# Optimization experiments

Hardware: AMD Instinct MI355X
Metric: run time of the kernel (lower is better)

The kernel has to match this reference:

```python
import jax, jax.numpy as jnp
import numpy as np

N, G, M = 3000, 1000, 4000  # cells, genes, decoder nodes (M = N + G)


def _gat(A, W, Wb, vt, vtb, vr, vrb, H):
    # One graphattention_layer. Torch recomputes relu(W @ H) three times; the
    # math is identical, so compute it once.
    Z = jax.nn.relu(H @ W.T + Wb)            # (n, out)
    s = (Z @ vt.T + vtb).T                   # (1, n) -- vkt scores
    r = (Z @ vr.T + vrb).T                   # (1, n) -- vkr scores
    Ms = A * s                               # column-wise scaling of A
    Mr = (A * r).T                           # row-wise scaling (transposed)
    Att = jax.nn.softmax(jax.nn.sigmoid(Ms + Mr), axis=-1)  # torch dim=1 default for 2D
    return Att @ Z                           # (n, out)


LAYER_DIMS = {"e1": (N, 512), "e2": (512, 256), "e3": (256, 64),
              "d1": (64, 256), "d2": (256, 512), "d3": (512, M), "d4": (512, G)}


def setup_inputs() -> dict:
    key = jax.random.key(0)
    ks = iter(jax.random.split(key, 64))
    def rn(shape, scale=1.0):
        return jax.random.normal(next(ks), shape, dtype=jnp.float32) * scale
    inp = {}
    inp["X"] = jax.random.uniform(next(ks), (N, N), dtype=jnp.float32)      # cell adjacency (encoder input)
    inp["A_enc"] = jax.random.uniform(next(ks), (N, N), dtype=jnp.float32)  # encoder adjM
    inp["A_dec"] = jax.random.uniform(next(ks), (M, M), dtype=jnp.float32)  # decoder adjM (N+G nodes)
    inp["gG"] = rn((64, G))                                                  # gene embeddings
    for name, (fi, fo) in LAYER_DIMS.items():
        inp[name + "_W"] = rn((fo, fi), 1.0 / np.sqrt(fi))
        inp[name + "_Wb"] = jnp.zeros((fo,), jnp.float32)
        inp[name + "_vt"] = rn((1, fo), 1.0 / np.sqrt(fo))
        inp[name + "_vtb"] = jnp.zeros((1,), jnp.float32)
        inp[name + "_vr"] = rn((1, fo), 1.0 / np.sqrt(fo))
        inp[name + "_vrb"] = jnp.zeros((1,), jnp.float32)
    return inp


def reference(X, A_enc, A_dec, gG,
              e1_W, e1_Wb, e1_vt, e1_vtb, e1_vr, e1_vrb,
              e2_W, e2_Wb, e2_vt, e2_vtb, e2_vr, e2_vrb,
              e3_W, e3_Wb, e3_vt, e3_vtb, e3_vr, e3_vrb,
              d1_W, d1_Wb, d1_vt, d1_vtb, d1_vr, d1_vrb,
              d2_W, d2_Wb, d2_vt, d2_vtb, d2_vr, d2_vrb,
              d3_W, d3_Wb, d3_vt, d3_vtb, d3_vr, d3_vrb,
              d4_W, d4_Wb, d4_vt, d4_vtb, d4_vr, d4_vrb):
    H1 = _gat(A_enc, e1_W, e1_Wb, e1_vt, e1_vtb, e1_vr, e1_vrb, X.T)
    H2 = _gat(A_enc, e2_W, e2_Wb, e2_vt, e2_vtb, e2_vr, e2_vrb, H1)
    H3 = _gat(A_enc, e3_W, e3_Wb, e3_vt, e3_vtb, e3_vr, e3_vrb, H2)
    Henc = H3.T                                  # (64, N)
    # decoder: stack gene embeddings, transpose to (M, 64)
    D = jnp.concatenate([gG, Henc], axis=1).T    # (M, 64)
    D1 = _gat(A_dec, d1_W, d1_Wb, d1_vt, d1_vtb, d1_vr, d1_vrb, D)
    D2 = _gat(A_dec, d2_W, d2_Wb, d2_vt, d2_vtb, d2_vr, d2_vrb, D1)
    cell = _gat(A_dec, d3_W, d3_Wb, d3_vt, d3_vtb, d3_vr, d3_vrb, D2)   # (M, M)
    gene = _gat(A_dec, d4_W, d4_Wb, d4_vt, d4_vtb, d4_vr, d4_vrb, D2)   # (M, G)
    return (cell, gene)
```

## Files before the change

kernel.cpp:

```cpp
#include <hip/hip_runtime.h>
#include <hip/hip_bf16.h>

using bf16 = __hip_bfloat16;
typedef __bf16 bf16x8 __attribute__((ext_vector_type(8)));
typedef __bf16 bf16x4 __attribute__((ext_vector_type(4)));
typedef float f32x4 __attribute__((ext_vector_type(4)));
typedef unsigned short u16x4 __attribute__((ext_vector_type(4)));

#define N_CELLS 3000
#define N_GENES 1000
#define M_NODES 4000
#define NP 3072
#define MP 4096

__device__ __forceinline__ float rdv(const void* p, size_t i, int isbf) {
    if (isbf) return (float)((const bf16*)p)[i];
    return ((const float*)p)[i];
}

__device__ __forceinline__ f32x4 load4g(const void* A, int n, int row, int col, int isbf) {
    f32x4 v = {0.f, 0.f, 0.f, 0.f};
    if (row < n) {
        if (col + 3 < n) {
            if (isbf) {
                const u16x4 u = *(const u16x4*)((const unsigned short*)A + (size_t)row * n + col);
                #pragma unroll
                for (int k = 0; k < 4; k++) v[k] = __uint_as_float(((unsigned)u[k]) << 16);
            } else {
                v = *(const f32x4*)((const float*)A + (size_t)row * n + col);
            }
        } else {
            #pragma unroll
            for (int k = 0; k < 4; k++)
                if (col + k < n) v[k] = rdv(A, (size_t)row * n + col + k, isbf);
        }
    }
    return v;
}

__device__ __forceinline__ f32x4 load4b(const bf16* A, int ld, int row, int col) {
    const u16x4 u = *(const u16x4*)((const unsigned short*)A + (size_t)row * ld + col);
    f32x4 v;
    #pragma unroll
    for (int k = 0; k < 4; k++) v[k] = __uint_as_float(((unsigned)u[k]) << 16);
    return v;
}

__device__ __forceinline__ void async_copy16(const bf16* g, bf16* l) {
    __builtin_amdgcn_global_load_lds((const __attribute__((address_space(1))) void*)g,
                                     (__attribute__((address_space(3))) void*)l,
                                     16, 0, 0);
}

__global__ void sniff_dtype(const unsigned int* __restrict__ X, int* __restrict__ flag)
{
    __shared__ int cnt[4];
    int t = threadIdx.x;
    int c = 0;
    for (int i = t; i < 2048; i += 256)
        if ((X[i] & 0xFFFFu) < 0x3F80u) c++;
    #pragma unroll
    for (int off = 32; off > 0; off >>= 1) c += __shfl_down(c, off);
    if ((t & 63) == 0) cnt[t >> 6] = c;
    __syncthreads();
    if (t == 0) flag[0] = (cnt[0] + cnt[1] + cnt[2] + cnt[3] > 1536) ? 1 : 0;
}

template<bool BIAS_ROW, bool SCALE_ROW, bool ATOMIC, bool SCORES, typename OutT>
__global__ __launch_bounds__(256, 2)
void gemm_nt(const bf16* __restrict__ A, int lda,
             const bf16* __restrict__ B, int ldb,
             const bf16* __restrict__ bias,
             const float* __restrict__ rsum,
             OutT* __restrict__ C, int ldc,
             int K, int mBound, int nBound,
             const void* __restrict__ vtp, const void* __restrict__ vrp,
             const int* __restrict__ flag, int oBase, int oBound,
             float* __restrict__ sAcc, float* __restrict__ rAcc)
{
    __shared__ __align__(16) bf16 As[2][128 * 32];
    __shared__ __align__(16) bf16 Bs[2][128 * 32];
    const int tid  = threadIdx.x;
    const int wave = tid >> 6;
    const int lane = tid & 63;

    const int orig = blockIdx.y * gridDim.x + blockIdx.x;
    int i0, j0;
    if (gridDim.x == 32 && gridDim.y == 32) {
        const int xcd = orig & 7, idx = orig >> 3;
        const int r = ((xcd >> 1) << 3) + (idx >> 4);
        const int c = ((xcd & 1) << 4) + (idx & 15);
        i0 = r * 128;
        j0 = c * 128;
    } else {
        const int nwg = gridDim.x * gridDim.y;
        const int q = nwg >> 3, rr = nwg & 7;
        const int xcd = orig & 7, idx = orig >> 3;
        const int swz = (xcd < rr ? xcd * (q + 1) : rr * (q + 1) + (xcd - rr) * q) + idx;
        i0 = (swz / gridDim.x) * 128;
        j0 = (swz % gridDim.x) * 128;
    }

    const int kSlice = K / gridDim.z;
    const int kBase  = blockIdx.z * kSlice;
    const int kEnd   = kBase + kSlice;

    const int srow = lane >> 2;
    const int sk   = (lane & 3) * 8;
    const bf16* gA0 = A + (size_t)(i0 + wave * 32 + srow) * lda + sk;
    const bf16* gA1 = gA0 + (size_t)16 * lda;
    const bf16* gB0 = B + (size_t)(j0 + wave * 32 + srow) * ldb + sk;
    const bf16* gB1 = gB0 + (size_t)16 * ldb;
    const int loA0 = (wave * 32) * 32;
    const int loA1 = (wave * 32 + 16) * 32;

    const int wm = (wave >> 1) * 64;
    const int wn = (wave & 1) * 64;
    const int fr = lane & 15;
    const int fk = (lane >> 4) * 8;

    f32x4 acc[4][4] = {};

    auto stage = [&](int buf, int kt) {
        async_copy16(gA0 + kt, &As[buf][loA0]);
        async_copy16(gA1 + kt, &As[buf][loA1]);
        async_copy16(gB0 + kt, &Bs[buf][loA0]);
        async_copy16(gB1 + kt, &Bs[buf][loA1]);
    };

    stage(0, kBase);
    __syncthreads();
    int cur = 0;

    for (int kt = kBase; kt < kEnd; kt += 32) {
        if (kt + 32 < kEnd) stage(cur ^ 1, kt + 32);

        bf16x8 af[4], bfv[4];
        #pragma unroll
        for (int t = 0; t < 4; t++) {
            af[t]  = *(const bf16x8*)&As[cur][(wm + t * 16 + fr) * 32 + fk];
            bfv[t] = *(const bf16x8*)&Bs[cur][(wn + t * 16 + fr) * 32 + fk];
        }
        #pragma unroll
        for (int mt = 0; mt < 4; mt++)
            #pragma unroll
            for (int nt = 0; nt < 4; nt++)
                acc[mt][nt] = __builtin_amdgcn_mfma_f32_16x16x32_bf16(
                    af[mt], bfv[nt], acc[mt][nt], 0, 0, 0);

        __syncthreads();
        cur ^= 1;
    }

    const int ci = (lane >> 4) * 4;
    const int cj = lane & 15;
    int isbf = 0;
    if constexpr (SCORES) isbf = flag[0];
    float ps[4] = {0.f, 0.f, 0.f, 0.f};
    float pr[4] = {0.f, 0.f, 0.f, 0.f};
    #pragma unroll
    for (int mt = 0; mt < 4; mt++) {
        #pragma unroll
        for (int rg = 0; rg < 4; rg++) {
            const int gi = i0 + wm + mt * 16 + ci + rg;
            if (gi >= mBound) continue;
            float bv = 0.f, rc = 1.f;
            if (BIAS_ROW) bv = (float)bias[gi];
            if (SCALE_ROW) {
                const float r_ = rsum[gi];
                rc = r_ > 0.f ? __builtin_amdgcn_rcpf(r_) : 0.f;
            }
            float vtv = 0.f, vrv = 0.f;
            if constexpr (SCORES) {
                if (gi < oBound) {
                    vtv = rdv(vtp, (size_t)(oBase + gi), isbf);
                    vrv = rdv(vrp, (size_t)(oBase + gi), isbf);
                }
            }
            #pragma unroll
            for (int nt = 0; nt < 4; nt++) {
                const int gj = j0 + wn + nt * 16 + cj;
                if (gj >= nBound) continue;
                float v = acc[mt][nt][rg];
                if (BIAS_ROW) { v += bv; v = v > 0.f ? v : 0.f; }
                if (SCALE_ROW) v *= rc;
                if constexpr (ATOMIC) {
                    atomicAdd((float*)&C[(size_t)gi * ldc + gj], v);
                } else {
                    C[(size_t)gi * ldc + gj] = (OutT)v;
                }
                if constexpr (SCORES) {
                    ps[nt] += v * vtv;
                    pr[nt] += v * vrv;
                }
            }
        }
    }
    if constexpr (SCORES) {
        #pragma unroll
        for (int nt = 0; nt < 4; nt++) {
            float p = ps[nt], r2 = pr[nt];
            p  += __shfl_down(p, 32);  p  += __shfl_down(p, 16);
            r2 += __shfl_down(r2, 32); r2 += __shfl_down(r2, 16);
            if (lane < 16) {
                const int gj = j0 + wn + nt * 16 + lane;
                if (gj < nBound) {
                    atomicAdd(&sAcc[gj], p);
                    atomicAdd(&rAcc[gj], r2);
                }
            }
        }
    }
}

__global__ void padcopy(const void* __restrict__ src, int r, int c,
                        bf16* __restrict__ dst, int rp, int cp,
                        const int* __restrict__ flag)
{
    const int isbf = flag[0];
    long idx = (long)blockIdx.x * 256 + threadIdx.x;
    if (idx >= (long)rp * cp) return;
    int i = (int)(idx / cp), j = (int)(idx % cp);
    float v = 0.f;
    if (i < r && j < c) v = rdv(src, (size_t)i * c + j, isbf);
    dst[idx] = (bf16)v;
}

struct PadSeg { const void* src; bf16* dst; int r, c, cp; long base; };
struct PadArgs { PadSeg seg[14]; long total; };
__global__ void padcopy_multi(PadArgs a, const int* __restrict__ flag)
{
    const int isbf = flag[0];
    long idx = (long)blockIdx.x * 256 + threadIdx.x;
    const long str = (long)gridDim.x * 256;
    for (; idx < a.total; idx += str) {
        int s = 0;
        #pragma unroll
        for (int k = 1; k < 14; k++) if (idx >= a.seg[k].base) s = k;
        const long loc = idx - a.seg[s].base;
        const int cp = a.seg[s].cp;
        const int i = (int)(loc / cp), j = (int)(loc % cp);
        float v = 0.f;
        if (i < a.seg[s].r && j < a.seg[s].c)
            v = rdv(a.seg[s].src, (size_t)i * a.seg[s].c + j, isbf);
        a.seg[s].dst[loc] = (bf16)v;
    }
}

__global__ void padcopy_T(const void* __restrict__ src, int n,
                          bf16* __restrict__ dst, int np,
                          const int* __restrict__ flag)
{
    __shared__ float t[32][33];
    const int isbf = flag[0];
    const int tx = threadIdx.x & 31;
    const int ty = threadIdx.x >> 5;
    const int i0 = blockIdx.y * 32;
    const int k0 = blockIdx.x * 32;
    #pragma unroll
    for (int q = 0; q < 4; q++) {
        int k = k0 + ty + q * 8;
        float v = 0.f;
        if (k < n && i0 + tx < n) v = rdv(src, (size_t)k * n + i0 + tx, isbf);
        t[ty + q * 8][tx] = v;
    }
    __syncthreads();
    #pragma unroll
    for (int q = 0; q < 4; q++) {
        int i = ty + q * 8;
        dst[(size_t)(i0 + i) * np + k0 + tx] = (bf16)t[tx][i];
    }
}

__global__ void zero_f32(float* __restrict__ p, int n)
{
    int i = blockIdx.x * 256 + threadIdx.x;
    if (i < n) p[i] = 0.f;
}

__global__ void zero_f32v(f32x4* __restrict__ p, long n4)
{
    long i = (long)blockIdx.x * 256 + threadIdx.x;
    const long str = (long)gridDim.x * 256;
    const f32x4 z = {0.f, 0.f, 0.f, 0.f};
    for (; i < n4; i += str) p[i] = z;
}

__global__ void f32_to_bf16_v4(const f32x4* __restrict__ src, bf16x4* __restrict__ dst, long n4)
{
    long i = (long)blockIdx.x * 256 + threadIdx.x;
    const long str = (long)gridDim.x * 256;
    for (; i < n4; i += str) {
        f32x4 v = src[i];
        bf16x4 w;
        #pragma unroll
        for (int k = 0; k < 4; k++) w[k] = (__bf16)v[k];
        dst[i] = w;
    }
}

template<bool CB>
__global__ __launch_bounds__(256)
void e_pass_pair(const void* __restrict__ A, int ldA, int n,
                 const float* __restrict__ s, const float* __restrict__ r,
                 const void* __restrict__ vtb, const void* __restrict__ vrb,
                 bf16* __restrict__ E, int ldE, float* __restrict__ rowsum,
                 const int* __restrict__ flag)
{
    extern __shared__ char smem[];
    const int bi = blockIdx.y, bj = blockIdx.x;
    if (bj < bi) return;
    const int isbf = flag[0];
    const int tid = threadIdx.x;
    const int i0 = bi * 64, j0 = bj * 64;
    const int tx = tid & 15;
    const int ty = tid >> 4;
    const int c0 = 4 * tx;
    const float bt = rdv(vtb, 0, isbf);
    const float br = rdv(vrb, 0, isbf);

    auto ld4 = [&](int row, int col) -> f32x4 {
        if constexpr (CB) return load4b((const bf16*)A, ldA, row, col);
        else              return load4g(A, n, row, col, isbf);
    };
    auto stT = [&](int which, int a, int b, float v) {
        if constexpr (CB) ((__bf16*)smem)[((which << 6) + a) * 66 + b] = (__bf16)v;
        else              ((float*)smem)[((which << 6) + a) * 65 + b] = v;
    };
    auto ldT = [&](int which, int a, int b) -> float {
        if constexpr (CB) return (float)((__bf16*)smem)[((which << 6) + a) * 66 + b];
        else              return ((float*)smem)[((which << 6) + a) * 65 + b];
    };

    #pragma unroll
    for (int rr = 0; rr < 4; rr++) {
        const int rw = ty + 16 * rr;
        f32x4 v1 = ld4(i0 + rw, j0 + c0);
        f32x4 v2 = ld4(j0 + rw, i0 + c0);
        #pragma unroll
        for (int k = 0; k < 4; k++) {
            stT(0, c0 + k, rw, v1[k]);
            stT(1, c0 + k, rw, v2[k]);
        }
    }
    __syncthreads();

    const float LOG2E = 1.442695041f;

    {
        f32x4 s4 = *(const f32x4*)&s[j0 + c0];
        #pragma unroll
        for (int k = 0; k < 4; k++) s4[k] += bt;
        #pragma unroll
        for (int q = 0; q < 4; q++) {
            const int li = ty + 16 * q;
            const int gi = i0 + li;
            const float rv = r[gi] + br;
            const f32x4 a = ld4(gi, j0 + c0);
            f32x4 ev;
            float part = 0.f;
            #pragma unroll
            for (int k = 0; k < 4; k++) {
                const float trn = ldT(1, li, c0 + k);
                const float x = a[k] * s4[k] + trn * rv;
                const float t = __builtin_amdgcn_exp2f(-x * LOG2E);
                const float sig = __builtin_amdgcn_rcpf(1.f + t);
                float e = __builtin_amdgcn_exp2f(sig * LOG2E);
                const int gj = j0 + c0 + k;
                e = (gi < n && gj < n) ? e : 0.f;
                ev[k] = e;
                part += e;
            }
            bf16x4 w;
            #pragma unroll
            for (int k = 0; k < 4; k++) w[k] = (__bf16)ev[k];
            *(bf16x4*)&E[(size_t)gi * ldE + j0 + c0] = w;
            part += __shfl_down(part, 8, 16);
            part += __shfl_down(part, 4, 16);
            part += __shfl_down(part, 2, 16);
            part += __shfl_down(part, 1, 16);
            if (tx == 0) atomicAdd(&rowsum[gi], part);
        }
    }

    if (bj > bi) {
        f32x4 s4 = *(const f32x4*)&s[i0 + c0];
        #pragma unroll
        for (int k = 0; k < 4; k++) s4[k] += bt;
        #pragma unroll
        for (int q = 0; q < 4; q++) {
            const int lr = ty + 16 * q;
            const int gr = j0 + lr;
            const float rv = r[gr] + br;
            const f32x4 a = ld4(gr, i0 + c0);
            f32x4 ev;
            float part = 0.f;
            #pragma unroll
            for (int k = 0; k < 4; k++) {
                const float trn = ldT(0, lr, c0 + k);
                const float x = a[k] * s4[k] + trn * rv;
                const float t = __builtin_amdgcn_exp2f(-x * LOG2E);
                const float sig = __builtin_amdgcn_rcpf(1.f + t);
                float e = __builtin_amdgcn_exp2f(sig * LOG2E);
                const int gj = i0 + c0 + k;
                e = (gr < n && gj < n) ? e : 0.f;
                ev[k] = e;
                part += e;
            }
            bf16x4 w;
            #pragma unroll
            for (int k = 0; k < 4; k++) w[k] = (__bf16)ev[k];
            *(bf16x4*)&E[(size_t)gr * ldE + i0 + c0] = w;
            part += __shfl_down(part, 8, 16);
            part += __shfl_down(part, 4, 16);
            part += __shfl_down(part, 2, 16);
            part += __shfl_down(part, 1, 16);
            if (tx == 0) atomicAdd(&rowsum[gr], part);
        }
    }
}

__global__ void build_D(const void* __restrict__ gG, const bf16* __restrict__ H3,
                        bf16* __restrict__ D, const int* __restrict__ flag)
{
    const int isbf = flag[0];
    int idx = blockIdx.x * 256 + threadIdx.x;
    int m = idx >> 7, c = idx & 127;
    float v = 0.f;
    if (c < 64) {
        if (m < N_GENES)      v = rdv(gG, (size_t)c * N_GENES + m, isbf);
        else if (m < M_NODES) v = (float)H3[(size_t)(m - N_GENES) * 128 + c];
    }
    D[idx] = (bf16)v;
}

extern "C" void kernel_launch(void* const* d_in, const int* in_sizes, int n_in,
                              void* d_out, int out_size, void* d_ws, size_t ws_size,
                              hipStream_t stream)
{
    const void* X     = d_in[0];
    const void* A_enc = d_in[1];
    const void* A_dec = d_in[2];
    const void* gG    = d_in[3];
    const void *W[7], *Wb[7], *vt[7], *vtb[7], *vr[7], *vrb[7];
    for (int l = 0; l < 7; l++) {
        W[l]   = d_in[4 + 6 * l + 0];
        Wb[l]  = d_in[4 + 6 * l + 1];
        vt[l]  = d_in[4 + 6 * l + 2];
        vtb[l] = d_in[4 + 6 * l + 3];
        vr[l]  = d_in[4 + 6 * l + 4];
        vrb[l] = d_in[4 + 6 * l + 5];
    }

    const int fop[7] = {512, 256, 128, 256, 512, 4096, 1024};
    const int fip[7] = {3072, 512, 256, 128, 256, 512, 512};
    const int foR[7] = {512, 256, 64, 256, 512, 4000, 1000};
    const int fiR[7] = {3000, 512, 256, 64, 256, 512, 512};

    const int  CHcap = (ws_size >= (size_t)100 * 1024 * 1024) ? 4096 : 1024;
    const bool useAB = (ws_size >= (size_t)130 * 1024 * 1024);

    char* ws = (char*)d_ws;
    size_t off = 0;
    auto alloc = [&](size_t bytes) -> void* {
        void* p = ws + off;
        off += (bytes + 255) & ~(size_t)255;
        return p;
    };
    int*   flag = (int*)alloc(256);
    float* sb   = (float*)alloc((size_t)MP * 4);
    float* rb   = (float*)alloc((size_t)MP * 4);
    float* rsum = (float*)alloc((size_t)MP * 4);
    bf16* Bp[7];
    for (int l = 0; l < 7; l++) Bp[l] = (bf16*)alloc((size_t)fop[l] * 2);
    bf16* RA = (bf16*)alloc((size_t)NP * 512 * 2);
    bf16* RB = (bf16*)alloc((size_t)NP * 256 * 2);
    bf16* RC = (bf16*)alloc((size_t)MP * 512 * 2);
    bf16 *H1 = RA, *H3 = RA, *D1 = RA;
    bf16 *H2 = RB, *Dd = RB;
    bf16 *D2 = RC;
    bf16* Wp[7];
    for (int l = 0; l < 7; l++) Wp[l] = (bf16*)alloc((size_t)fop[l] * fip[l] * 2);
    float* Hf = (float*)alloc((size_t)MP * 512 * 4);
    bf16*  ZT = (bf16*)alloc((size_t)CHcap * MP * 2);
    bf16*  E  = (bf16*)alloc((size_t)MP * MP * 2);
    bf16*  Ab = useAB ? (bf16*)alloc((size_t)MP * MP * 2) : nullptr;
    bf16* XT = E;

    auto pickS = [](int base, int Kc) -> int {
        if (base >= 192) return 1;
        const int steps = Kc / 32;
        int best = 1;
        for (int S = 1; S <= 16; S++) {
            if (steps % S) continue;
            if (Kc / S < 256) continue;
            if (base * S > 1536) break;
            best = S;
            if (base * S >= 768) break;
        }
        return best;
    };

    sniff_dtype<<<1, 256, 0, stream>>>((const unsigned int*)X, flag);
    {
        PadArgs pa;
        long base = 0;
        for (int l = 0; l < 7; l++) {
            pa.seg[l] = {W[l], Wp[l], foR[l], fiR[l], fip[l], base};
            base += (long)fop[l] * fip[l];
        }
        for (int l = 0; l < 7; l++) {
            pa.seg[7 + l] = {Wb[l], Bp[l], 1, foR[l], fop[l], base};
            base += fop[l];
        }
        pa.total = base;
        padcopy_multi<<<2048, 256, 0, stream>>>(pa, flag);
    }
    padcopy_T<<<dim3(NP / 32, NP / 32), 256, 0, stream>>>(X, N_CELLS, XT, NP, flag);
    if (useAB)
        padcopy<<<dim3((NP * NP) / 256), 256, 0, stream>>>(
            A_enc, N_CELLS, N_CELLS, Ab, NP, NP, flag);

    const unsigned smemCB = 2 * 64 * 66 * 2;
    const unsigned smemF  = 2 * 64 * 65 * 4;

    auto layer = [&](const bf16* Hin, int l, const void* Araw, int nABpad,
                     int nReal, int nPad, bf16* HoutB, float* HoutF,
                     int ldOut, int mB, int nBtot) {
        const int K = fip[l], NO = fop[l];
        const int CH = NO > CHcap ? CHcap : NO;
        const int nch = NO / CH;
        auto gemm1 = [&](int c, bool withScores) {
            int sB = foR[l] - c * CH;
            if (sB > CH) sB = CH;
            if (sB < 0) sB = 0;
            if (withScores)
                gemm_nt<true, false, false, true, bf16><<<dim3(nPad / 128, CH / 128), 256, 0, stream>>>(
                    Wp[l] + (size_t)c * CH * K, K, Hin, K, Bp[l] + c * CH, nullptr,
                    ZT, nPad, K, CH, nPad,
                    vt[l], vr[l], flag, c * CH, sB, sb, rb);
            else
                gemm_nt<true, false, false, false, bf16><<<dim3(nPad / 128, CH / 128), 256, 0, stream>>>(
                    Wp[l] + (size_t)c * CH * K, K, Hin, K, Bp[l] + c * CH, nullptr,
                    ZT, nPad, K, CH, nPad,
                    nullptr, nullptr, nullptr, 0, 0, nullptr, nullptr);
        };
        zero_f32<<<dim3(3 * MP / 256), 256, 0, stream>>>(sb, 3 * MP);
        for (int c = 0; c < nch; c++) gemm1(c, true);
        if (useAB)
            e_pass_pair<true><<<dim3(nPad / 64, nPad / 64), 256, smemCB, stream>>>(
                Ab, nABpad, nReal, sb, rb, vtb[l], vrb[l], E, nPad, rsum, flag);
        else
            e_pass_pair<false><<<dim3(nPad / 64, nPad / 64), 256, smemF, stream>>>(
                Araw, nReal, nReal, sb, rb, vtb[l], vrb[l], E, nPad, rsum, flag);
        if (HoutB)
            zero_f32v<<<2048, 256, 0, stream>>>((f32x4*)Hf, (long)nPad * nBtot / 4);
        for (int c = 0; c < nch; c++) {
            if (nch > 1) gemm1(c, false);
            int colBase = c * CH;
            int nB = nBtot - colBase;
            if (nB > CH) nB = CH;
            if (nB <= 0) continue;
            const int bx = CH / 128, by = nPad / 128;
            if (HoutB) {
                const int S = pickS(bx * by, nPad);
                gemm_nt<false, true, true, false, float><<<dim3(bx, by, S), 256, 0, stream>>>(
                    E, nPad, ZT, nPad, nullptr, rsum,
                    Hf + colBase, nBtot, nPad, nPad, nB,
                    nullptr, nullptr, nullptr, 0, 0, nullptr, nullptr);
            } else {
                const int S = (nch == 1 && bx * by == 256) ? 2 : 1;
                if (S == 2) {
                    zero_f32v<<<2048, 256, 0, stream>>>(
                        (f32x4*)HoutF, (long)mB * ldOut / 4);
                    gemm_nt<false, true, true, false, float><<<dim3(bx, by, S), 256, 0, stream>>>(
                        E, nPad, ZT, nPad, nullptr, rsum,
                        HoutF + colBase, ldOut, nPad, mB, nB,
                        nullptr, nullptr, nullptr, 0, 0, nullptr, nullptr);
                } else {
                    gemm_nt<false, true, false, false, float><<<dim3(bx, by), 256, 0, stream>>>(
                        E, nPad, ZT, nPad, nullptr, rsum,
                        HoutF + colBase, ldOut, nPad, mB, nB,
                        nullptr, nullptr, nullptr, 0, 0, nullptr, nullptr);
                }
            }
        }
        if (HoutB)
            f32_to_bf16_v4<<<2048, 256, 0, stream>>>(
                (const f32x4*)Hf, (bf16x4*)HoutB, (long)nPad * nBtot / 4);
    };

    layer(XT,      0, A_enc, NP, N_CELLS, NP, H1, nullptr, 512, NP, 512);
    layer(H1,      1, A_enc, NP, N_CELLS, NP, H2, nullptr, 256, NP, 256);
    layer(H2,      2, A_enc, NP, N_CELLS, NP, H3, nullptr, 128, NP, 128);
    build_D<<<dim3((MP * 128) / 256), 256, 0, stream>>>(gG, H3, Dd, flag);
    if (useAB)
        padcopy<<<dim3((int)(((long)MP * MP) / 256)), 256, 0, stream>>>(
            A_dec, M_NODES, M_NODES, Ab, MP, MP, flag);
    layer(Dd, 3, A_dec, MP, M_NODES, MP, D1, nullptr, 256, MP, 256);
    layer(D1, 4, A_dec, MP, M_NODES, MP, D2, nullptr, 512, MP, 512);
    float* outCell = (float*)d_out;
    float* outGene = outCell + (size_t)M_NODES * M_NODES;
    layer(D2, 5, A_dec, MP, M_NODES, MP, nullptr, outCell, 4000, 4000, 4000);
    layer(D2, 6, A_dec, MP, M_NODES, MP, nullptr, outGene, 1000, 4000, 1000);
}
```

Measured before the change: 1.208 ms.

## Add 64x64-tile projection GEMM, fuse Hf zeroing into conversion, tune split-K

Adds a smaller 64x64-tile MFMA GEMM with XCD-aware block swizzle, used for the first (projection) GEMM when the output chunk is at most 512 wide. This raises block counts for the small-width layers and should improve CU occupancy. The per-layer zeroing of the float accumulator is removed. Instead the accumulator is zeroed once up front and re-zeroed inside the f32-to-bf16 conversion pass, which saves one full-buffer write pass per layer. The split-K heuristic now stops at a lower block-count threshold, which trades parallelism for fewer atomics.

```diff
diff --git a/kernel.cpp b/kernel.cpp
--- a/kernel.cpp
+++ b/kernel.cpp
@@ -213,6 +213,124 @@
     }
 }
 
+template<bool SCORES>
+__global__ __launch_bounds__(256, 4)
+void gemm1_64(const bf16* __restrict__ A, int lda,
+              const bf16* __restrict__ B, int ldb,
+              const bf16* __restrict__ bias,
+              bf16* __restrict__ C, int ldc,
+              int K, int mBound, int nBound,
+              const void* __restrict__ vtp, const void* __restrict__ vrp,
+              const int* __restrict__ flag, int oBase, int oBound,
+              float* __restrict__ sAcc, float* __restrict__ rAcc)
+{
+    __shared__ __align__(16) bf16 As[2][64 * 32];
+    __shared__ __align__(16) bf16 Bs[2][64 * 32];
+    const int tid  = threadIdx.x;
+    const int wave = tid >> 6;
+    const int lane = tid & 63;
+
+    const int nwg = gridDim.x * gridDim.y;
+    const int orig = blockIdx.y * gridDim.x + blockIdx.x;
+    const int q = nwg >> 3, rr = nwg & 7;
+    const int xcd = orig & 7, idx = orig >> 3;
+    const int swz = (xcd < rr ? xcd * (q + 1) : rr * (q + 1) + (xcd - rr) * q) + idx;
+    const int i0 = (swz / gridDim.x) * 64;
+    const int j0 = (swz % gridDim.x) * 64;
+
+    const int srow = lane >> 2;
+    const int sk   = (lane & 3) * 8;
+    const bf16* gA = A + (size_t)(i0 + wave * 16 + srow) * lda + sk;
+    const bf16* gB = B + (size_t)(j0 + wave * 16 + srow) * ldb + sk;
+    const int lo = wave * 16 * 32;
+
+    const int wm = (wave >> 1) * 32;
+    const int wn = (wave & 1) * 32;
+    const int fr = lane & 15;
+    const int fk = (lane >> 4) * 8;
+
+    f32x4 acc[2][2] = {};
+
+    auto stage = [&](int buf, int kt) {
+        async_copy16(gA + kt, &As[buf][lo]);
+        async_copy16(gB + kt, &Bs[buf][lo]);
+    };
+
+    stage(0, 0);
+    __syncthreads();
+    int cur = 0;
+
+    for (int kt = 0; kt < K; kt += 32) {
+        if (kt + 32 < K) stage(cur ^ 1, kt + 32);
+
+        bf16x8 af[2], bfv[2];
+        #pragma unroll
+        for (int t = 0; t < 2; t++) {
+            af[t]  = *(const bf16x8*)&As[cur][(wm + t * 16 + fr) * 32 + fk];
+            bfv[t] = *(const bf16x8*)&Bs[cur][(wn + t * 16 + fr) * 32 + fk];
+        }
+        #pragma unroll
+        for (int mt = 0; mt < 2; mt++)
+            #pragma unroll
+            for (int nt = 0; nt < 2; nt++)
+                acc[mt][nt] = __builtin_amdgcn_mfma_f32_16x16x32_bf16(
+                    af[mt], bfv[nt], acc[mt][nt], 0, 0, 0);
+
+        __syncthreads();
+        cur ^= 1;
+    }
+
+    const int ci = (lane >> 4) * 4;
+    const int cj = lane & 15;
+    int isbf = 0;
+    if constexpr (SCORES) isbf = flag[0];
+    float ps[2] = {0.f, 0.f};
+    float pr[2] = {0.f, 0.f};
+    #pragma unroll
+    for (int mt = 0; mt < 2; mt++) {
+        #pragma unroll
+        for (int rg = 0; rg < 4; rg++) {
+            const int gi = i0 + wm + mt * 16 + ci + rg;
+            if (gi >= mBound) continue;
+            const float bv = (float)bias[gi];
+            float vtv = 0.f, vrv = 0.f;
+            if constexpr (SCORES) {
+                if (gi < oBound) {
+                    vtv = rdv(vtp, (size_t)(oBase + gi), isbf);
+                    vrv = rdv(vrp, (size_t)(oBase + gi), isbf);
+                }
+            }
+            #pragma unroll
+            for (int nt = 0; nt < 2; nt++) {
+                const int gj = j0 + wn + nt * 16 + cj;
+                if (gj >= nBound) continue;
+                float v = acc[mt][nt][rg] + bv;
+                v = v > 0.f ? v : 0.f;
+                C[(size_t)gi * ldc + gj] = (bf16)v;
+                if constexpr (SCORES) {
+                    ps[nt] += v * vtv;
+                    pr[nt] += v * vrv;
+                }
+            }
+        }
+    }
+    if constexpr (SCORES) {
+        #pragma unroll
+        for (int nt = 0; nt < 2; nt++) {
+            float p = ps[nt], r2 = pr[nt];
+            p  += __shfl_down(p, 32);  p  += __shfl_down(p, 16);
+            r2 += __shfl_down(r2, 32); r2 += __shfl_down(r2, 16);
+            if (lane < 16) {
+                const int gj = j0 + wn + nt * 16 + lane;
+                if (gj < nBound) {
+                    atomicAdd(&sAcc[gj], p);
+                    atomicAdd(&rAcc[gj], r2);
+                }
+            }
+        }
+    }
+}
+
 __global__ void padcopy(const void* __restrict__ src, int r, int c,
                         bf16* __restrict__ dst, int rp, int cp,
                         const int* __restrict__ flag)
@@ -286,12 +404,14 @@
     for (; i < n4; i += str) p[i] = z;
 }
 
-__global__ void f32_to_bf16_v4(const f32x4* __restrict__ src, bf16x4* __restrict__ dst, long n4)
+__global__ void f32_to_bf16_zero(f32x4* __restrict__ src, bf16x4* __restrict__ dst, long n4)
 {
     long i = (long)blockIdx.x * 256 + threadIdx.x;
     const long str = (long)gridDim.x * 256;
+    const f32x4 z = {0.f, 0.f, 0.f, 0.f};
     for (; i < n4; i += str) {
         f32x4 v = src[i];
+        src[i] = z;
         bf16x4 w;
         #pragma unroll
         for (int k = 0; k < 4; k++) w[k] = (__bf16)v[k];
@@ -496,7 +616,7 @@
             if (Kc / S < 256) continue;
             if (base * S > 1536) break;
             best = S;
-            if (base * S >= 768) break;
+            if (base * S >= 384) break;
         }
         return best;
     };
@@ -517,6 +637,7 @@
         padcopy_multi<<<2048, 256, 0, stream>>>(pa, flag);
     }
     padcopy_T<<<dim3(NP / 32, NP / 32), 256, 0, stream>>>(X, N_CELLS, XT, NP, flag);
+    zero_f32v<<<2048, 256, 0, stream>>>((f32x4*)Hf, (long)MP * 512);
     if (useAB)
         padcopy<<<dim3((NP * NP) / 256), 256, 0, stream>>>(
             A_enc, N_CELLS, N_CELLS, Ab, NP, NP, flag);
@@ -534,16 +655,28 @@
             int sB = foR[l] - c * CH;
             if (sB > CH) sB = CH;
             if (sB < 0) sB = 0;
-            if (withScores)
-                gemm_nt<true, false, false, true, bf16><<<dim3(nPad / 128, CH / 128), 256, 0, stream>>>(
-                    Wp[l] + (size_t)c * CH * K, K, Hin, K, Bp[l] + c * CH, nullptr,
-                    ZT, nPad, K, CH, nPad,
-                    vt[l], vr[l], flag, c * CH, sB, sb, rb);
-            else
-                gemm_nt<true, false, false, false, bf16><<<dim3(nPad / 128, CH / 128), 256, 0, stream>>>(
-                    Wp[l] + (size_t)c * CH * K, K, Hin, K, Bp[l] + c * CH, nullptr,
-                    ZT, nPad, K, CH, nPad,
-                    nullptr, nullptr, nullptr, 0, 0, nullptr, nullptr);
+            const bf16* Aw = Wp[l] + (size_t)c * CH * K;
+            if (CH <= 512) {
+                if (withScores)
+                    gemm1_64<true><<<dim3(nPad / 64, CH / 64), 256, 0, stream>>>(
+                        Aw, K, Hin, K, Bp[l] + c * CH, ZT, nPad, K, CH, nPad,
+                        vt[l], vr[l], flag, c * CH, sB, sb, rb);
+                else
+                    gemm1_64<false><<<dim3(nPad / 64, CH / 64), 256, 0, stream>>>(
+                        Aw, K, Hin, K, Bp[l] + c * CH, ZT, nPad, K, CH, nPad,
+                        nullptr, nullptr, nullptr, 0, 0, nullptr, nullptr);
+            } else {
+                if (withScores)
+                    gemm_nt<true, false, false, true, bf16><<<dim3(nPad / 128, CH / 128), 256, 0, stream>>>(
+                        Aw, K, Hin, K, Bp[l] + c * CH, nullptr,
+                        ZT, nPad, K, CH, nPad,
+                        vt[l], vr[l], flag, c * CH, sB, sb, rb);
+                else
+                    gemm_nt<true, false, false, false, bf16><<<dim3(nPad / 128, CH / 128), 256, 0, stream>>>(
+                        Aw, K, Hin, K, Bp[l] + c * CH, nullptr,
+                        ZT, nPad, K, CH, nPad,
+                        nullptr, nullptr, nullptr, 0, 0, nullptr, nullptr);
+            }
         };
         zero_f32<<<dim3(3 * MP / 256), 256, 0, stream>>>(sb, 3 * MP);
         for (int c = 0; c < nch; c++) gemm1(c, true);
@@ -553,8 +686,6 @@
         else
             e_pass_pair<false><<<dim3(nPad / 64, nPad / 64), 256, smemF, stream>>>(
                 Araw, nReal, nReal, sb, rb, vtb[l], vrb[l], E, nPad, rsum, flag);
-        if (HoutB)
-            zero_f32v<<<2048, 256, 0, stream>>>((f32x4*)Hf, (long)nPad * nBtot / 4);
         for (int c = 0; c < nch; c++) {
             if (nch > 1) gemm1(c, false);
             int colBase = c * CH;
@@ -586,8 +717,8 @@
             }
         }
         if (HoutB)
-            f32_to_bf16_v4<<<2048, 256, 0, stream>>>(
-                (const f32x4*)Hf, (bf16x4*)HoutB, (long)nPad * nBtot / 4);
+            f32_to_bf16_zero<<<2048, 256, 0, stream>>>(
+                (f32x4*)Hf, (bf16x4*)HoutB, (long)nPad * nBtot / 4);
     };
 
     layer(XT,      0, A_enc, NP, N_CELLS, NP, H1, nullptr, 512, NP, 512);
```

After: 1.082 ms. 10.5% less time.
